# Performance work log

Hardware: AMD Instinct MI355X
Metric: run time of the kernel (lower is better)

Reference implementation:

```python
import jax, jax.numpy as jnp
import numpy as np

NEG_SLOPE = 0.2  # PyG GATConv default LeakyReLU slope
EPS = 1e-16
LN_EPS = 1e-5


def setup_inputs() -> dict:
    key = jax.random.key(0)
    ks = jax.random.split(key, 12)
    N, E, HID, H = 10000, 320000, 256, 4
    C = HID // H
    s = 1.0 / np.sqrt(HID)
    x = jax.random.normal(ks[0], (N, HID), jnp.float32)
    src = jax.random.randint(ks[1], (E,), 0, N, dtype=jnp.int32)
    dst = jax.random.randint(ks[2], (E,), 0, N, dtype=jnp.int32)
    edge_index = jnp.stack([src, dst])
    edge_attr = jax.random.normal(ks[3], (E, 1), jnp.float32)
    W = jax.random.normal(ks[4], (HID, HID), jnp.float32) * s
    att_src = jax.random.normal(ks[5], (H, C), jnp.float32) * s
    att_dst = jax.random.normal(ks[6], (H, C), jnp.float32) * s
    We = jax.random.normal(ks[7], (1, HID), jnp.float32) * s
    att_edge = jax.random.normal(ks[8], (H, C), jnp.float32) * s
    bias = jnp.zeros((HID,), jnp.float32)
    gamma = jnp.ones((HID,), jnp.float32)
    beta = jnp.zeros((HID,), jnp.float32)
    return {"x": x, "edge_index": edge_index, "edge_attr": edge_attr, "W": W,
            "att_src": att_src, "att_dst": att_dst, "We": We,
            "att_edge": att_edge, "bias": bias, "gamma": gamma, "beta": beta}


def _gat_layer(x, edge_index, edge_attr, W, att_src, att_dst, We, att_edge,
               bias, gamma, beta):
    N, HID = x.shape
    H, C = att_src.shape
    src, dst = edge_index[0], edge_index[1]

    # add_self_loops=True with fill_value='mean': self-loop edge_attr is the
    # mean of incoming edge features per node (0 if no incoming edges).
    ones = jnp.ones((src.shape[0],), x.dtype)
    deg = jax.ops.segment_sum(ones, dst, num_segments=N)
    loop_attr = jax.ops.segment_sum(edge_attr, dst, num_segments=N) \
        / jnp.maximum(deg, 1.0)[:, None]
    loop_idx = jnp.arange(N, dtype=src.dtype)
    src = jnp.concatenate([src, loop_idx])
    dst = jnp.concatenate([dst, loop_idx])
    e_attr = jnp.concatenate([edge_attr, loop_attr], axis=0)  # [E+N, 1]

    # node / edge projections
    xp = (x @ W).reshape(N, H, C)                 # [N,H,C]
    a_s = jnp.einsum('nhc,hc->nh', xp, att_src)   # [N,H]
    a_d = jnp.einsum('nhc,hc->nh', xp, att_dst)
    ep = (e_attr @ We).reshape(-1, H, C)          # [E+N,H,C]
    a_e = jnp.einsum('ehc,hc->eh', ep, att_edge)  # [E+N,H]

    logits = a_s[src] + a_d[dst] + a_e            # [E+N,H]
    logits = jax.nn.leaky_relu(logits, NEG_SLOPE)

    # segment softmax over destination neighborhoods
    m = jax.ops.segment_max(logits, dst, num_segments=N)    # [N,H]
    p = jnp.exp(logits - m[dst])
    z = jax.ops.segment_sum(p, dst, num_segments=N)         # [N,H]
    alpha = p / (z[dst] + EPS)                              # [E+N,H]

    # gather-weight-scatter messages
    msg = xp[src] * alpha[:, :, None]                       # [E+N,H,C]
    out = jax.ops.segment_sum(msg, dst, num_segments=N)     # [N,H,C]
    out = out.reshape(N, H * C) + bias

    # LayerNorm (per node over features) + residual + ReLU (dropout in eval)
    mu = jnp.mean(out, axis=-1, keepdims=True)
    var = jnp.var(out, axis=-1, keepdims=True)
    h = (out - mu) * jax.lax.rsqrt(var + LN_EPS) * gamma + beta
    return jax.nn.relu(h + x)


def reference(x, edge_index, edge_attr, W, att_src, att_dst, We, att_edge,
              bias, gamma, beta):
    return _gat_layer(x, edge_index, edge_attr, W, att_src, att_dst, We,
                      att_edge, bias, gamma, beta)
```

## Files before the change

kernel.cpp:

```cpp
#include <hip/hip_runtime.h>

#define HID 256
#define NH 4
#define NEG 0.2f
#define SUBSTRIDE 24
#define NODESTRIDE 192

typedef __attribute__((ext_vector_type(8))) short short8;
typedef __attribute__((ext_vector_type(4))) float f32x4;

__device__ __forceinline__ unsigned short f2b(float f) {
    unsigned u = __float_as_uint(f);
    u = u + 0x7FFFu + ((u >> 16) & 1u);
    return (unsigned short)(u >> 16);
}
__device__ __forceinline__ float b2f_lo(unsigned u) {
    return __uint_as_float(u << 16);
}
__device__ __forceinline__ float b2f_hi(unsigned u) {
    return __uint_as_float(u & 0xFFFF0000u);
}
__device__ __forceinline__ float lrelu(float f) {
    return f > 0.f ? f : NEG * f;
}

__global__ __launch_bounds__(256) void k_init(
    const float* __restrict__ x, const float* __restrict__ W,
    const float* __restrict__ We, const float* __restrict__ att_edge,
    unsigned short* __restrict__ Ap, unsigned short* __restrict__ Bp,
    float* __restrict__ wedot, int* __restrict__ deg8, int N, int ZB,
    int XB) {
    __shared__ unsigned short sm[4096];
    int b = blockIdx.x, t = threadIdx.x;
    if (b < ZB) {
        int i = b * 256 + t;
        if (i < N * 2) ((int4*)deg8)[i] = make_int4(0, 0, 0, 0);
        return;
    }
    int b2 = b - ZB;
    if (b2 < XB) {
        int fi = b2;
        int r = t >> 4;
        int row = fi * 16 + r;
        const float4* x4 = (const float4*)x;
        #pragma unroll
        for (int q = 0; q < 4; q++) {
            int c4 = (t & 15) + (q << 4);
            unsigned u0 = 0, u1 = 0;
            if (row < N) {
                float4 v = x4[(size_t)row * 64 + c4];
                u0 = (unsigned)f2b(v.x) | ((unsigned)f2b(v.y) << 16);
                u1 = (unsigned)f2b(v.z) | ((unsigned)f2b(v.w) << 16);
            }
            int k0 = c4 << 2;
            int ks = k0 >> 5, ko = k0 & 31;
            int lane = r + ((ko >> 3) << 4);
            int off = ks * 512 + lane * 8 + (ko & 7);
            *((uint2*)&sm[off]) = make_uint2(u0, u1);
        }
        __syncthreads();
        uint4* out = (uint4*)(Ap + (size_t)fi * 4096);
        const uint4* smv = (const uint4*)sm;
        out[t] = smv[t];
        out[256 + t] = smv[256 + t];
    } else if (b2 < XB + 16) {
        int n16 = b2 - XB;
        int k = t;
        int ks = k >> 5;
        int lhi = ((k & 31) >> 3) << 4;
        int j = k & 7;
        const float4* W4 = (const float4*)W;
        #pragma unroll
        for (int q = 0; q < 4; q++) {
            float4 v = W4[(size_t)k * 64 + n16 * 4 + q];
            int c = q << 2;
            sm[ks * 512 + (lhi + c + 0) * 8 + j] = f2b(v.x);
            sm[ks * 512 + (lhi + c + 1) * 8 + j] = f2b(v.y);
            sm[ks * 512 + (lhi + c + 2) * 8 + j] = f2b(v.z);
            sm[ks * 512 + (lhi + c + 3) * 8 + j] = f2b(v.w);
        }
        __syncthreads();
        uint4* out = (uint4*)(Bp + (size_t)n16 * 4096);
        const uint4* smv = (const uint4*)sm;
        out[t] = smv[t];
        out[256 + t] = smv[256 + t];
    } else {
        float v = We[t] * att_edge[t];
        #pragma unroll
        for (int off = 32; off; off >>= 1) v += __shfl_down(v, off);
        if ((t & 63) == 0) wedot[t >> 6] = v;
    }
}

__global__ __launch_bounds__(256) void k_capmm(
    const int* __restrict__ src, const int* __restrict__ dst,
    const float* __restrict__ eattr,
    const unsigned short* __restrict__ Ap, const unsigned short* __restrict__ Bp,
    const float* __restrict__ att_src, const float* __restrict__ att_dst,
    unsigned short* __restrict__ xp, float* __restrict__ a_s,
    float* __restrict__ a_d, int* __restrict__ deg8, int2* __restrict__ adj,
    int N, int E, int DBc, int MF) {
    int t = threadIdx.x;
    if ((int)blockIdx.x < DBc) {
        int base = blockIdx.x * 1024 + t;
        #pragma unroll
        for (int q = 0; q < 4; q++) {
            int e = base + q * 256;
            if (e < E) {
                int d = dst[e];
                int sub = e & 7;
                int p = atomicAdd(&deg8[(d << 3) | sub], 1);
                if (p < SUBSTRIDE)
                    adj[(size_t)d * NODESTRIDE + sub * SUBSTRIDE + p] =
                        make_int2(src[e], __float_as_int(eattr[e]));
            }
        }
        return;
    }
    int w = t >> 6, l = t & 63;
    int fi0 = (blockIdx.x - DBc) * 4;
    const short8* A8 = (const short8*)Ap;
    const short8* B8 = (const short8*)Bp;
    f32x4 acc[4][4];
    #pragma unroll
    for (int mi = 0; mi < 4; mi++)
        #pragma unroll
        for (int ni = 0; ni < 4; ni++)
            acc[mi][ni] = (f32x4){0.f, 0.f, 0.f, 0.f};
    short8 zz = {0, 0, 0, 0, 0, 0, 0, 0};
    #pragma unroll
    for (int ks = 0; ks < 8; ks++) {
        short8 a[4], b[4];
        #pragma unroll
        for (int mi = 0; mi < 4; mi++) {
            int fi = fi0 + mi;
            a[mi] = (fi < MF) ? A8[(size_t)(fi * 8 + ks) * 64 + l] : zz;
        }
        #pragma unroll
        for (int ni = 0; ni < 4; ni++)
            b[ni] = B8[(size_t)(((w << 2) + ni) * 8 + ks) * 64 + l];
        #pragma unroll
        for (int mi = 0; mi < 4; mi++)
            #pragma unroll
            for (int ni = 0; ni < 4; ni++)
                acc[mi][ni] = __builtin_amdgcn_mfma_f32_16x16x32_bf16(
                    a[mi], b[ni], acc[mi][ni], 0, 0, 0);
    }
    int colb = w << 6;
    float asc[4], adc[4];
    #pragma unroll
    for (int ni = 0; ni < 4; ni++) {
        asc[ni] = att_src[colb + ni * 16 + (l & 15)];
        adc[ni] = att_dst[colb + ni * 16 + (l & 15)];
    }
    #pragma unroll
    for (int mi = 0; mi < 4; mi++) {
        int rowb = fi0 * 16 + mi * 16 + ((l >> 4) << 2);
        #pragma unroll
        for (int r = 0; r < 4; r++) {
            int row = rowb + r;
            float ps = 0.f, pd = 0.f;
            #pragma unroll
            for (int ni = 0; ni < 4; ni++) {
                float v = acc[mi][ni][r];
                ps += v * asc[ni];
                pd += v * adc[ni];
            }
            #pragma unroll
            for (int off = 1; off < 16; off <<= 1) {
                ps += __shfl_xor(ps, off);
                pd += __shfl_xor(pd, off);
            }
            if (row < N) {
                if ((l & 15) == 0) {
                    a_s[(row << 2) + w] = ps;
                    a_d[(row << 2) + w] = pd;
                }
                #pragma unroll
                for (int ni = 0; ni < 4; ni++)
                    xp[(size_t)row * HID + colb + ni * 16 + (l & 15)] =
                        f2b(acc[mi][ni][r]);
            }
        }
    }
}

__global__ __launch_bounds__(256) void k_gather_ln(
    const int2* __restrict__ adj, const int* __restrict__ deg8,
    const float4* __restrict__ a_s4, const float4* __restrict__ a_d4,
    const float* __restrict__ wedot, const unsigned short* __restrict__ xp,
    const float4* __restrict__ x4, const float4* __restrict__ bias4,
    const float4* __restrict__ gamma4, const float4* __restrict__ beta4,
    float4* __restrict__ out4, int N) {
    __shared__ float4 sp[4][64];
    int t = threadIdx.x;
    int u = t >> 6, l = t & 63, hl = l >> 4;
    int n = blockIdx.x * 4 + u;
    if (n >= N) return;
    int vsub = (l < 8) ? deg8[(n << 3) + l] : 0;
    int pre[9];
    pre[0] = 0;
    #pragma unroll
    for (int k = 0; k < 8; k++) pre[k + 1] = pre[k] + __shfl(vsub, k);
    int cnt = pre[8];
    const int2* adjn = adj + (size_t)n * NODESTRIDE;
    float4 adn = a_d4[n];
    float4 wh = *(const float4*)wedot;
    float4 zl = {0.f, 0.f, 0.f, 0.f};
    float sel = 0.f;
    float acc0 = 0.f, acc1 = 0.f, acc2 = 0.f, acc3 = 0.f;
    int ntile = (cnt + 63) >> 6;
    for (int tile = 0; tile < ntile; tile++) {
        int j = (tile << 6) + l;
        float4 p = {0.f, 0.f, 0.f, 0.f};
        float ea = 0.f;
        int s = 0;
        if (j < cnt) {
            int kk = 0, prek = 0;
            #pragma unroll
            for (int q = 1; q < 8; q++) {
                int ge = (j >= pre[q]);
                kk += ge;
                prek = ge ? pre[q] : prek;
            }
            int2 a = adjn[kk * SUBSTRIDE + (j - prek)];
            s = a.x;
            ea = __int_as_float(a.y);
            float4 as_ = a_s4[s];
            p.x = __expf(lrelu(as_.x + adn.x + ea * wh.x));
            p.y = __expf(lrelu(as_.y + adn.y + ea * wh.y));
            p.z = __expf(lrelu(as_.z + adn.z + ea * wh.z));
            p.w = __expf(lrelu(as_.w + adn.w + ea * wh.w));
        }
        zl.x += p.x;
        zl.y += p.y;
        zl.z += p.z;
        zl.w += p.w;
        sel += ea;
        sp[u][l] = p;
        const float* spf = (const float*)&sp[u][0];
        int lim = min(64, cnt - (tile << 6));
        int jj = 0;
        for (; jj + 8 <= lim; jj += 8) {
            int s_[8];
            float p_[8];
            uint2 r_[8];
            #pragma unroll
            for (int k = 0; k < 8; k++)
                s_[k] = __builtin_amdgcn_readfirstlane(__shfl(s, jj + k));
            #pragma unroll
            for (int k = 0; k < 8; k++) {
                p_[k] = spf[(jj + k) * 4 + hl];
                r_[k] = *(const uint2*)(xp + (size_t)s_[k] * HID + 4 * l);
            }
            #pragma unroll
            for (int k = 0; k < 8; k++) {
                acc0 += p_[k] * b2f_lo(r_[k].x);
                acc1 += p_[k] * b2f_hi(r_[k].x);
                acc2 += p_[k] * b2f_lo(r_[k].y);
                acc3 += p_[k] * b2f_hi(r_[k].y);
            }
        }
        for (; jj < lim; jj++) {
            int sj = __builtin_amdgcn_readfirstlane(__shfl(s, jj));
            float pj = spf[jj * 4 + hl];
            uint2 r = *(const uint2*)(xp + (size_t)sj * HID + 4 * l);
            acc0 += pj * b2f_lo(r.x);
            acc1 += pj * b2f_hi(r.x);
            acc2 += pj * b2f_lo(r.y);
            acc3 += pj * b2f_hi(r.y);
        }
    }
    #pragma unroll
    for (int off = 32; off; off >>= 1) {
        zl.x += __shfl_xor(zl.x, off);
        zl.y += __shfl_xor(zl.y, off);
        zl.z += __shfl_xor(zl.z, off);
        zl.w += __shfl_xor(zl.w, off);
        sel += __shfl_xor(sel, off);
    }
    float loop_ea = sel / fmaxf((float)cnt, 1.0f);
    float4 asn = a_s4[n];
    float4 pf;
    pf.x = __expf(lrelu(asn.x + adn.x + loop_ea * wh.x));
    pf.y = __expf(lrelu(asn.y + adn.y + loop_ea * wh.y));
    pf.z = __expf(lrelu(asn.z + adn.z + loop_ea * wh.z));
    pf.w = __expf(lrelu(asn.w + adn.w + loop_ea * wh.w));
    zl.x += pf.x;
    zl.y += pf.y;
    zl.z += pf.z;
    zl.w += pf.w;
    float psl = hl < 2 ? (hl == 0 ? pf.x : pf.y) : (hl == 2 ? pf.z : pf.w);
    uint2 rv = *(const uint2*)(xp + (size_t)n * HID + 4 * l);
    acc0 += psl * b2f_lo(rv.x);
    acc1 += psl * b2f_hi(rv.x);
    acc2 += psl * b2f_lo(rv.y);
    acc3 += psl * b2f_hi(rv.y);
    float zh = hl < 2 ? (hl == 0 ? zl.x : zl.y) : (hl == 2 ? zl.z : zl.w);
    float zi = 1.0f / (zh + 1e-16f);
    float4 bi = bias4[l];
    float v0 = acc0 * zi + bi.x;
    float v1 = acc1 * zi + bi.y;
    float v2 = acc2 * zi + bi.z;
    float v3 = acc3 * zi + bi.w;
    float s1 = v0 + v1 + v2 + v3;
    float s2 = v0 * v0 + v1 * v1 + v2 * v2 + v3 * v3;
    #pragma unroll
    for (int off = 32; off; off >>= 1) {
        s1 += __shfl_xor(s1, off);
        s2 += __shfl_xor(s2, off);
    }
    float mu = s1 * (1.0f / HID);
    float var = s2 * (1.0f / HID) - mu * mu;
    float rstd = rsqrtf(var + 1e-5f);
    float4 g = gamma4[l], be = beta4[l], xr = x4[(size_t)n * 64 + l];
    float4 o;
    o.x = (v0 - mu) * rstd * g.x + be.x + xr.x;
    o.y = (v1 - mu) * rstd * g.y + be.y + xr.y;
    o.z = (v2 - mu) * rstd * g.z + be.z + xr.z;
    o.w = (v3 - mu) * rstd * g.w + be.w + xr.w;
    o.x = o.x > 0.f ? o.x : 0.f;
    o.y = o.y > 0.f ? o.y : 0.f;
    o.z = o.z > 0.f ? o.z : 0.f;
    o.w = o.w > 0.f ? o.w : 0.f;
    out4[(size_t)n * 64 + l] = o;
}

extern "C" void kernel_launch(void* const* d_in, const int* in_sizes, int n_in,
                              void* d_out, int out_size, void* d_ws,
                              size_t ws_size, hipStream_t stream) {
    const float* x        = (const float*)d_in[0];
    const int*   ei       = (const int*)d_in[1];
    const float* eattr    = (const float*)d_in[2];
    const float* W        = (const float*)d_in[3];
    const float* att_src  = (const float*)d_in[4];
    const float* att_dst  = (const float*)d_in[5];
    const float* We       = (const float*)d_in[6];
    const float* att_edge = (const float*)d_in[7];
    const float* bias     = (const float*)d_in[8];
    const float* gamma    = (const float*)d_in[9];
    const float* beta     = (const float*)d_in[10];

    int N = in_sizes[0] / HID;
    int E = in_sizes[1] / 2;
    const int* src = ei;
    const int* dst = ei + E;

    int MF = (N + 15) / 16;
    size_t NP = (size_t)MF * 16;

    float* base = (float*)d_ws;
    unsigned short* Ap = (unsigned short*)base;
    unsigned short* Bp = (unsigned short*)(base + NP * 128);
    unsigned short* xp = (unsigned short*)(base + NP * 128 + 32768);
    float* a_s    = base + NP * 256 + 32768;
    float* a_d    = a_s + (size_t)N * 4;
    float* wedot  = a_d + (size_t)N * 4;
    int* deg8     = (int*)(wedot + 8);
    int2* adj     = (int2*)(deg8 + (size_t)N * 8);

    int ZB = (N * 2 + 255) / 256;
    int XB = MF;
    k_init<<<ZB + XB + 17, 256, 0, stream>>>(x, W, We, att_edge, Ap, Bp,
                                             wedot, deg8, N, ZB, XB);

    int DBc = (E + 1023) / 1024;
    int MB = (MF + 3) / 4;
    k_capmm<<<DBc + MB, 256, 0, stream>>>(src, dst, eattr, Ap, Bp, att_src,
                                          att_dst, xp, a_s, a_d, deg8, adj, N,
                                          E, DBc, MF);

    k_gather_ln<<<(N + 3) / 4, 256, 0, stream>>>(
        adj, deg8, (const float4*)a_s, (const float4*)a_d, wedot, xp,
        (const float4*)x, (const float4*)bias, (const float4*)gamma,
        (const float4*)beta, (float4*)d_out, N);
}
```

Baseline: 57.71 us.

## Fuse x bf16 conversion into GEMM kernel via shared-memory staging

```diff
diff --git a/kernel.cpp b/kernel.cpp
--- a/kernel.cpp
+++ b/kernel.cpp
@@ -25,11 +25,9 @@
 }
 
 __global__ __launch_bounds__(256) void k_init(
-    const float* __restrict__ x, const float* __restrict__ W,
-    const float* __restrict__ We, const float* __restrict__ att_edge,
-    unsigned short* __restrict__ Ap, unsigned short* __restrict__ Bp,
-    float* __restrict__ wedot, int* __restrict__ deg8, int N, int ZB,
-    int XB) {
+    const float* __restrict__ W, const float* __restrict__ We,
+    const float* __restrict__ att_edge, unsigned short* __restrict__ Bp,
+    float* __restrict__ wedot, int* __restrict__ deg8, int N, int ZB) {
     __shared__ unsigned short sm[4096];
     int b = blockIdx.x, t = threadIdx.x;
     if (b < ZB) {
@@ -38,33 +36,8 @@
         return;
     }
     int b2 = b - ZB;
-    if (b2 < XB) {
-        int fi = b2;
-        int r = t >> 4;
-        int row = fi * 16 + r;
-        const float4* x4 = (const float4*)x;
-        #pragma unroll
-        for (int q = 0; q < 4; q++) {
-            int c4 = (t & 15) + (q << 4);
-            unsigned u0 = 0, u1 = 0;
-            if (row < N) {
-                float4 v = x4[(size_t)row * 64 + c4];
-                u0 = (unsigned)f2b(v.x) | ((unsigned)f2b(v.y) << 16);
-                u1 = (unsigned)f2b(v.z) | ((unsigned)f2b(v.w) << 16);
-            }
-            int k0 = c4 << 2;
-            int ks = k0 >> 5, ko = k0 & 31;
-            int lane = r + ((ko >> 3) << 4);
-            int off = ks * 512 + lane * 8 + (ko & 7);
-            *((uint2*)&sm[off]) = make_uint2(u0, u1);
-        }
-        __syncthreads();
-        uint4* out = (uint4*)(Ap + (size_t)fi * 4096);
-        const uint4* smv = (const uint4*)sm;
-        out[t] = smv[t];
-        out[256 + t] = smv[256 + t];
-    } else if (b2 < XB + 16) {
-        int n16 = b2 - XB;
+    if (b2 < 16) {
+        int n16 = b2;
         int k = t;
         int ks = k >> 5;
         int lhi = ((k & 31) >> 3) << 4;
@@ -94,17 +67,17 @@
 
 __global__ __launch_bounds__(256) void k_capmm(
     const int* __restrict__ src, const int* __restrict__ dst,
-    const float* __restrict__ eattr,
-    const unsigned short* __restrict__ Ap, const unsigned short* __restrict__ Bp,
-    const float* __restrict__ att_src, const float* __restrict__ att_dst,
-    unsigned short* __restrict__ xp, float* __restrict__ a_s,
-    float* __restrict__ a_d, int* __restrict__ deg8, int2* __restrict__ adj,
-    int N, int E, int DBc, int MF) {
+    const float* __restrict__ eattr, const float* __restrict__ x,
+    const unsigned short* __restrict__ Bp, const float* __restrict__ att_src,
+    const float* __restrict__ att_dst, unsigned short* __restrict__ xp,
+    float* __restrict__ a_s, float* __restrict__ a_d, int* __restrict__ deg8,
+    int2* __restrict__ adj, int N, int E, int DBc, int MF) {
+    __shared__ unsigned short smA[16384];
     int t = threadIdx.x;
     if ((int)blockIdx.x < DBc) {
-        int base = blockIdx.x * 1024 + t;
-        #pragma unroll
-        for (int q = 0; q < 4; q++) {
+        int base = blockIdx.x * 2048 + t;
+        #pragma unroll
+        for (int q = 0; q < 8; q++) {
             int e = base + q * 256;
             if (e < E) {
                 int d = dst[e];
@@ -117,9 +90,32 @@
         }
         return;
     }
+    int fi0 = (blockIdx.x - DBc) * 4;
+    {
+        int r = t >> 4;
+        const float4* x4 = (const float4*)x;
+        #pragma unroll
+        for (int mi = 0; mi < 4; mi++) {
+            int row = (fi0 + mi) * 16 + r;
+            #pragma unroll
+            for (int q = 0; q < 4; q++) {
+                int c4 = (t & 15) + (q << 4);
+                unsigned u0 = 0, u1 = 0;
+                if (row < N) {
+                    float4 v = x4[(size_t)row * 64 + c4];
+                    u0 = (unsigned)f2b(v.x) | ((unsigned)f2b(v.y) << 16);
+                    u1 = (unsigned)f2b(v.z) | ((unsigned)f2b(v.w) << 16);
+                }
+                int k0 = c4 << 2;
+                int ks = k0 >> 5, ko = k0 & 31;
+                int lane = r + ((ko >> 3) << 4);
+                int off = mi * 4096 + ks * 512 + lane * 8 + (ko & 7);
+                *((uint2*)&smA[off]) = make_uint2(u0, u1);
+            }
+        }
+    }
+    __syncthreads();
     int w = t >> 6, l = t & 63;
-    int fi0 = (blockIdx.x - DBc) * 4;
-    const short8* A8 = (const short8*)Ap;
     const short8* B8 = (const short8*)Bp;
     f32x4 acc[4][4];
     #pragma unroll
@@ -127,15 +123,12 @@
         #pragma unroll
         for (int ni = 0; ni < 4; ni++)
             acc[mi][ni] = (f32x4){0.f, 0.f, 0.f, 0.f};
-    short8 zz = {0, 0, 0, 0, 0, 0, 0, 0};
     #pragma unroll
     for (int ks = 0; ks < 8; ks++) {
         short8 a[4], b[4];
         #pragma unroll
-        for (int mi = 0; mi < 4; mi++) {
-            int fi = fi0 + mi;
-            a[mi] = (fi < MF) ? A8[(size_t)(fi * 8 + ks) * 64 + l] : zz;
-        }
+        for (int mi = 0; mi < 4; mi++)
+            a[mi] = *(const short8*)&smA[mi * 4096 + (ks * 64 + l) * 8];
         #pragma unroll
         for (int ni = 0; ni < 4; ni++)
             b[ni] = B8[(size_t)(((w << 2) + ni) * 8 + ks) * 64 + l];
@@ -350,23 +343,21 @@
     size_t NP = (size_t)MF * 16;
 
     float* base = (float*)d_ws;
-    unsigned short* Ap = (unsigned short*)base;
-    unsigned short* Bp = (unsigned short*)(base + NP * 128);
-    unsigned short* xp = (unsigned short*)(base + NP * 128 + 32768);
-    float* a_s    = base + NP * 256 + 32768;
+    unsigned short* Bp = (unsigned short*)base;
+    unsigned short* xp = (unsigned short*)(base + 32768);
+    float* a_s    = base + 32768 + NP * 128;
     float* a_d    = a_s + (size_t)N * 4;
     float* wedot  = a_d + (size_t)N * 4;
     int* deg8     = (int*)(wedot + 8);
     int2* adj     = (int2*)(deg8 + (size_t)N * 8);
 
     int ZB = (N * 2 + 255) / 256;
-    int XB = MF;
-    k_init<<<ZB + XB + 17, 256, 0, stream>>>(x, W, We, att_edge, Ap, Bp,
-                                             wedot, deg8, N, ZB, XB);
-
-    int DBc = (E + 1023) / 1024;
+    k_init<<<ZB + 17, 256, 0, stream>>>(W, We, att_edge, Bp, wedot, deg8, N,
+                                        ZB);
+
+    int DBc = (E + 2047) / 2048;
     int MB = (MF + 3) / 4;
-    k_capmm<<<DBc + MB, 256, 0, stream>>>(src, dst, eattr, Ap, Bp, att_src,
+    k_capmm<<<DBc + MB, 256, 0, stream>>>(src, dst, eattr, x, Bp, att_src,
                                           att_dst, xp, a_s, a_d, deg8, adj, N,
                                           E, DBc, MF);
 
```

After: 54.69 us (median of 4 runs). -5.2%, faster.
